# Performance work log

Hardware: AMD Instinct MI355X
Metric: run time of the kernel (lower is better)

## Reference

```python
import jax, jax.numpy as jnp
import numpy as np

D = 256          # d_model
NH = 8           # heads
NP = 4           # points per level
NL = 4           # feature levels
DH = D // NH     # head dim = 32
MLP = 4 * D      # 1024
B = 2
SHAPES = [(128, 128), (64, 64), (32, 32), (16, 16)]
LQ = sum(h * w for h, w in SHAPES)  # 21760
EPS = 1e-6


def layer_norm(x, g, b):
    mu = jnp.mean(x, axis=-1, keepdims=True)
    var = jnp.mean(jnp.square(x - mu), axis=-1, keepdims=True)
    return (x - mu) * jax.lax.rsqrt(var + EPS) * g + b


def bilinear_sample(val_l, loc, Hs, Ws):
    # val_l: [B, Hs*Ws, NH, DH]; loc: [B, Lq, NH, NP, 2] normalized in [0,1]
    v = val_l.transpose(0, 2, 1, 3)                      # [B, NH, HW, DH]
    x = loc[..., 0] * Ws - 0.5                           # [B, Lq, NH, NP]
    y = loc[..., 1] * Hs - 0.5
    x0 = jnp.floor(x); y0 = jnp.floor(y)
    lx = x - x0; ly = y - y0
    x0i = x0.astype(jnp.int32); y0i = y0.astype(jnp.int32)

    def gather(xi, yi):
        inb = (xi >= 0) & (xi < Ws) & (yi >= 0) & (yi < Hs)
        idx = jnp.clip(yi, 0, Hs - 1) * Ws + jnp.clip(xi, 0, Ws - 1)
        idx = idx.transpose(0, 2, 1, 3)                  # [B, NH, Lq, NP]
        sh = idx.shape
        idxf = idx.reshape(sh[0], sh[1], -1)
        g = jax.vmap(jax.vmap(lambda vv, ii: vv[ii]))(v, idxf)
        g = g.reshape(sh[0], sh[1], sh[2], sh[3], v.shape[-1])
        return g * inb.transpose(0, 2, 1, 3)[..., None].astype(g.dtype)

    wt = lambda a: a.transpose(0, 2, 1, 3)[..., None]    # -> [B, NH, Lq, NP, 1]
    out = (gather(x0i, y0i) * wt((1 - lx) * (1 - ly))
           + gather(x0i + 1, y0i) * wt(lx * (1 - ly))
           + gather(x0i, y0i + 1) * wt((1 - lx) * ly)
           + gather(x0i + 1, y0i + 1) * wt(lx * ly))
    return out                                            # [B, NH, Lq, NP, DH]


def setup_inputs() -> dict:
    key = jax.random.key(0)
    ks = jax.random.split(key, 16)
    ss = np.array(SHAPES, dtype=np.int64)
    lsi = np.concatenate([[0], np.cumsum(ss[:, 0] * ss[:, 1])[:-1]]).astype(np.int64)
    s = 0.02
    return {
        'src': jax.random.normal(ks[0], (B, LQ, D), jnp.float32),
        'pos': jax.random.normal(ks[1], (B, LQ, D), jnp.float32),
        'reference_points': jax.random.uniform(ks[2], (B, LQ, NL, 2), jnp.float32),
        'spatial_shapes': ss,
        'level_start_index': lsi,
        'g1': jnp.ones((D,), jnp.float32), 'beta1': jnp.zeros((D,), jnp.float32),
        'w_off': jax.random.normal(ks[3], (D, NH * NL * NP * 2), jnp.float32) * 0.01,
        'b_off': jax.random.normal(ks[4], (NH * NL * NP * 2,), jnp.float32) * 0.1,
        'w_attn': jax.random.normal(ks[5], (D, NH * NL * NP), jnp.float32) * s,
        'b_attn': jnp.zeros((NH * NL * NP,), jnp.float32),
        'w_val': jax.random.normal(ks[6], (D, D), jnp.float32) * s,
        'b_val': jnp.zeros((D,), jnp.float32),
        'w_out': jax.random.normal(ks[7], (D, D), jnp.float32) * s,
        'b_out': jnp.zeros((D,), jnp.float32),
        'g2': jnp.ones((D,), jnp.float32), 'beta2': jnp.zeros((D,), jnp.float32),
        'w_fc1': jax.random.normal(ks[8], (D, MLP), jnp.float32) * s,
        'b_fc1': jnp.zeros((MLP,), jnp.float32),
        'w_fc2': jax.random.normal(ks[9], (MLP, D), jnp.float32) * s,
        'b_fc2': jnp.zeros((D,), jnp.float32),
    }


def reference(src, pos, reference_points, spatial_shapes, level_start_index,
              g1, beta1, w_off, b_off, w_attn, b_attn, w_val, b_val,
              w_out, b_out, g2, beta2, w_fc1, b_fc1, w_fc2, b_fc2):
    ss = np.asarray(spatial_shapes)
    lsi = np.asarray(level_start_index)
    Bsz, Lq, _ = src.shape

    # --- pre-norm + multi-scale deformable attention + residual ---
    x = layer_norm(src, g1, beta1)
    q = x + pos
    val = (x @ w_val + b_val).reshape(Bsz, Lq, NH, DH)
    off = (q @ w_off + b_off).reshape(Bsz, Lq, NH, NL, NP, 2)
    aw = jax.nn.softmax((q @ w_attn + b_attn).reshape(Bsz, Lq, NH, NL * NP), axis=-1)
    aw = aw.reshape(Bsz, Lq, NH, NL, NP)

    out = jnp.zeros((Bsz, Lq, NH, DH), src.dtype)
    for l in range(NL):
        Hs, Ws = int(ss[l, 0]), int(ss[l, 1])
        start = int(lsi[l])
        vl = val[:, start:start + Hs * Ws]                       # [B, HW, NH, DH]
        norm = jnp.array([Ws, Hs], src.dtype)
        loc = reference_points[:, :, None, l, None, :] + off[:, :, :, l] / norm
        samp = bilinear_sample(vl, loc, Hs, Ws)                  # [B, NH, Lq, NP, DH]
        a = aw[:, :, :, l].transpose(0, 2, 1, 3)                 # [B, NH, Lq, NP]
        out = out + jnp.einsum('bhqp,bhqpd->bqhd', a, samp)
    attn_out = out.reshape(Bsz, Lq, D) @ w_out + b_out
    src2 = src + attn_out

    # --- pre-norm MLP + residual ---
    y = layer_norm(src2, g2, beta2)
    ffn = jax.nn.relu(y @ w_fc1 + b_fc1) @ w_fc2 + b_fc2
    return src2 + ffn
```

## Files before the change

### kernel.cpp

```cpp
#include <hip/hip_runtime.h>

#define DMODEL 256
#define NHEAD 8
#define NPOINT 4
#define NLEVEL 4
#define DHEAD 32
#define MLPD 1024
#define BSZ 2
#define LQTOK 21760
#define NTOK (BSZ * LQTOK)
#define LNEPS 1e-6f
#define FFN_CHUNK 21760

typedef __attribute__((ext_vector_type(8))) short short8;
typedef __attribute__((ext_vector_type(4))) float f32x4;

__device__ __forceinline__ float bf2f(unsigned short u) {
  unsigned int i = ((unsigned int)u) << 16;
  return __builtin_bit_cast(float, i);
}
__device__ __forceinline__ unsigned short f2bf(float f) {
  unsigned int i = __builtin_bit_cast(unsigned int, f);
  i += 0x7fff + ((i >> 16) & 1);
  return (unsigned short)(i >> 16);
}
__device__ __forceinline__ float bflo(unsigned int u) {
  return __builtin_bit_cast(float, u << 16);
}
__device__ __forceinline__ float bfhi(unsigned int u) {
  return __builtin_bit_cast(float, u & 0xffff0000u);
}

__device__ __forceinline__ void gload_lds16(const unsigned short* g,
                                            unsigned short* lds) {
  __builtin_amdgcn_global_load_lds(
      (const __attribute__((address_space(1))) unsigned int*)g,
      (__attribute__((address_space(3))) unsigned int*)lds, 16, 0, 0);
}

template <bool EMITQ>
__global__ __launch_bounds__(256) void ln_bf16(
    const float* __restrict__ in, const float* __restrict__ g,
    const float* __restrict__ beta, unsigned short* __restrict__ o,
    const float* __restrict__ pos, unsigned short* __restrict__ q) {
  const int w = threadIdx.x >> 6, lane = threadIdx.x & 63;
  const size_t t = (size_t)blockIdx.x * 4 + w;
  const size_t base = t * DMODEL + lane * 4;
  float4 v = *(const float4*)(in + base);
  float s = (v.x + v.y) + (v.z + v.w);
#pragma unroll
  for (int off = 32; off; off >>= 1) s += __shfl_xor(s, off, 64);
  float mu = s * (1.0f / DMODEL);
  float dx = v.x - mu, dy = v.y - mu, dz = v.z - mu, dw = v.w - mu;
  float s2 = (dx * dx + dy * dy) + (dz * dz + dw * dw);
#pragma unroll
  for (int off = 32; off; off >>= 1) s2 += __shfl_xor(s2, off, 64);
  float rs = rsqrtf(s2 * (1.0f / DMODEL) + LNEPS);
  float4 gg = *(const float4*)(g + lane * 4);
  float4 bb = *(const float4*)(beta + lane * 4);
  unsigned short r0 = f2bf(dx * rs * gg.x + bb.x);
  unsigned short r1 = f2bf(dy * rs * gg.y + bb.y);
  unsigned short r2 = f2bf(dz * rs * gg.z + bb.z);
  unsigned short r3 = f2bf(dw * rs * gg.w + bb.w);
  unsigned int lo = ((unsigned int)r1 << 16) | r0;
  unsigned int hi = ((unsigned int)r3 << 16) | r2;
  *(uint2*)(o + base) = make_uint2(lo, hi);
  if (EMITQ) {
    float4 p = *(const float4*)(pos + base);
    unsigned short q0 = f2bf(bf2f(r0) + p.x);
    unsigned short q1 = f2bf(bf2f(r1) + p.y);
    unsigned short q2 = f2bf(bf2f(r2) + p.z);
    unsigned short q3 = f2bf(bf2f(r3) + p.w);
    unsigned int ql = ((unsigned int)q1 << 16) | q0;
    unsigned int qh = ((unsigned int)q3 << 16) | q2;
    *(uint2*)(q + base) = make_uint2(ql, qh);
  }
}

__global__ __launch_bounds__(256) void transpose_bf16(const float* __restrict__ W,
                                                      unsigned short* __restrict__ Wt,
                                                      int K, int N) {
  __shared__ float tile[32][33];
  int k0 = blockIdx.x * 32, n0 = blockIdx.y * 32;
  int tx = threadIdx.x & 31, ty = threadIdx.x >> 5;
  for (int i = ty; i < 32; i += 8) tile[i][tx] = W[(size_t)(k0 + i) * N + n0 + tx];
  __syncthreads();
  for (int i = ty; i < 32; i += 8)
    Wt[(size_t)(n0 + i) * K + k0 + tx] = f2bf(tile[tx][i]);
}

template <int OMODE>
__global__ __launch_bounds__(256) void gemm_mfma(
    const unsigned short* __restrict__ A, const unsigned short* __restrict__ Wt,
    const float* __restrict__ bias, const float* __restrict__ res,
    void* __restrict__ Cout, int M, int N, int K) {
  __shared__ __attribute__((aligned(16))) unsigned short As[128 * 32];
  __shared__ __attribute__((aligned(16))) unsigned short Bs[128 * 32];
  const int tid = threadIdx.x;
  const int m0 = blockIdx.x * 128, n0 = blockIdx.y * 128;
  const int wave = tid >> 6, lane = tid & 63;
  const int wm = (wave & 1) * 64, wn = (wave >> 1) * 64;
  const int lr = lane & 15, quad = lane >> 4;
  f32x4 acc[4][4] = {};
  for (int k0 = 0; k0 < K; k0 += 32) {
    __syncthreads();
#pragma unroll
    for (int r = 0; r < 2; r++) {
      int c = r * 256 + tid;
      int row = c >> 2, col8 = (c & 3) * 8;
      gload_lds16(Wt + (size_t)(n0 + row) * K + k0 + col8,
                  &Bs[(r * 256 + wave * 64) * 8]);
    }
#pragma unroll
    for (int r = 0; r < 2; r++) {
      int c = r * 256 + tid;
      int row = c >> 2, col8 = (c & 3) * 8;
      gload_lds16(A + (size_t)(m0 + row) * K + k0 + col8,
                  &As[(r * 256 + wave * 64) * 8]);
    }
    __syncthreads();
    short8 af[4], bfr[4];
#pragma unroll
    for (int i = 0; i < 4; i++)
      af[i] = *(const short8*)(&As[(wm + i * 16 + lr) * 32 + quad * 8]);
#pragma unroll
    for (int j = 0; j < 4; j++)
      bfr[j] = *(const short8*)(&Bs[(wn + j * 16 + lr) * 32 + quad * 8]);
#pragma unroll
    for (int i = 0; i < 4; i++)
#pragma unroll
      for (int j = 0; j < 4; j++)
        acc[i][j] = __builtin_amdgcn_mfma_f32_16x16x32_bf16(af[i], bfr[j],
                                                            acc[i][j], 0, 0, 0);
  }
#pragma unroll
  for (int i = 0; i < 4; i++) {
    int rbase = m0 + wm + i * 16 + quad * 4;
#pragma unroll
    for (int j = 0; j < 4; j++) {
      int col = n0 + wn + j * 16 + lr;
      float bv = bias[col];
#pragma unroll
      for (int r = 0; r < 4; r++) {
        size_t idx = (size_t)(rbase + r) * N + col;
        float v = acc[i][j][r] + bv;
        if (OMODE == 2) v = fmaxf(v, 0.0f);
        if (OMODE == 3) v += res[idx];
        if (OMODE == 3)
          ((float*)Cout)[idx] = v;
        else
          ((unsigned short*)Cout)[idx] = f2bf(v);
      }
    }
  }
}

__global__ __launch_bounds__(256) void deform_sample(
    const unsigned short* __restrict__ val, const unsigned short* __restrict__ off,
    const unsigned short* __restrict__ logits, const float* __restrict__ refp,
    unsigned short* __restrict__ out) {
  __shared__ __attribute__((aligned(16))) int sIdx[4][16][8][4];
  __shared__ __attribute__((aligned(16))) float sW[4][16][8][4];
  const int w = threadIdx.x >> 6, lane = threadIdx.x & 63;
  const int bq = blockIdx.x * 4 + w;
  const int b = bq / LQTOK;
  {
    const int HW_[4] = {128, 64, 32, 16};
    const int LSI_[4] = {0, 16384, 20480, 21504};
    int u0 = 2 * lane;
    int h = u0 >> 4;
    int lvl = (u0 >> 2) & 3;
    int pt0 = u0 & 15;
    int HW = HW_[lvl];
    float2 rp = ((const float2*)refp)[(size_t)bq * 4 + lvl];
    uint2 ov = *(const uint2*)(off + (size_t)bq * 256 + 4 * lane);
    unsigned int lgu = *(const unsigned int*)(logits + (size_t)bq * 128 + 2 * lane);
    float lg0 = bflo(lgu), lg1 = bfhi(lgu);
    float mx = fmaxf(lg0, lg1);
#pragma unroll
    for (int s = 1; s < 8; s <<= 1) mx = fmaxf(mx, __shfl_xor(mx, s, 64));
    float e0 = expf(lg0 - mx), e1 = expf(lg1 - mx);
    float es = e0 + e1;
#pragma unroll
    for (int s = 1; s < 8; s <<= 1) es += __shfl_xor(es, s, 64);
    float inv = 1.0f / es;
    float a01[2] = {e0 * inv, e1 * inv};
    unsigned int ovv[2] = {ov.x, ov.y};
    int hb = h * DHEAD;
#pragma unroll
    for (int c = 0; c < 2; c++) {
      float x = fmaf(rp.x, (float)HW, bflo(ovv[c])) - 0.5f;
      float y = fmaf(rp.y, (float)HW, bfhi(ovv[c])) - 0.5f;
      float xf = floorf(x), yf = floorf(y);
      int x0 = (int)xf, y0 = (int)yf;
      float lx = x - xf, ly = y - yf;
      int x0c = min(max(x0, 0), HW - 1);
      int x1c = min(max(x0 + 1, 0), HW - 1);
      int y0c = min(max(y0, 0), HW - 1);
      int y1c = min(max(y0 + 1, 0), HW - 1);
      float m0x = (x0 >= 0 && x0 < HW) ? 1.f : 0.f;
      float m1x = (x0 + 1 >= 0 && x0 + 1 < HW) ? 1.f : 0.f;
      float m0y = (y0 >= 0 && y0 < HW) ? 1.f : 0.f;
      float m1y = (y0 + 1 >= 0 && y0 + 1 < HW) ? 1.f : 0.f;
      float a = a01[c];
      int* ip = sIdx[w][pt0 + c][h];
      float* wp = sW[w][pt0 + c][h];
      ip[0] = (LSI_[lvl] + y0c * HW + x0c) * DMODEL + hb;
      ip[1] = (LSI_[lvl] + y0c * HW + x1c) * DMODEL + hb;
      ip[2] = (LSI_[lvl] + y1c * HW + x0c) * DMODEL + hb;
      ip[3] = (LSI_[lvl] + y1c * HW + x1c) * DMODEL + hb;
      wp[0] = (1.f - lx) * (1.f - ly) * m0x * m0y * a;
      wp[1] = lx * (1.f - ly) * m1x * m0y * a;
      wp[2] = (1.f - lx) * ly * m0x * m1y * a;
      wp[3] = lx * ly * m1x * m1y * a;
    }
  }
  __builtin_amdgcn_wave_barrier();
  const int h2 = lane >> 3, g = lane & 7;
  const unsigned short* vb = val + (size_t)b * LQTOK * DMODEL + g * 4;
  float a0 = 0.f, a1 = 0.f, a2 = 0.f, a3 = 0.f;
#pragma unroll
  for (int pb = 0; pb < 4; pb++) {
    int4 ix[4];
    float4 wt[4];
#pragma unroll
    for (int p = 0; p < 4; p++) {
      ix[p] = *(const int4*)sIdx[w][pb * 4 + p][h2];
      wt[p] = *(const float4*)sW[w][pb * 4 + p][h2];
    }
    uint2 v4[4][4];
#pragma unroll
    for (int p = 0; p < 4; p++) {
      v4[p][0] = *(const uint2*)(vb + ix[p].x);
      v4[p][1] = *(const uint2*)(vb + ix[p].y);
      v4[p][2] = *(const uint2*)(vb + ix[p].z);
      v4[p][3] = *(const uint2*)(vb + ix[p].w);
    }
#pragma unroll
    for (int p = 0; p < 4; p++) {
      float wk[4] = {wt[p].x, wt[p].y, wt[p].z, wt[p].w};
#pragma unroll
      for (int k = 0; k < 4; k++) {
        uint2 u = v4[p][k];
        a0 = fmaf(wk[k], bflo(u.x), a0);
        a1 = fmaf(wk[k], bfhi(u.x), a1);
        a2 = fmaf(wk[k], bflo(u.y), a2);
        a3 = fmaf(wk[k], bfhi(u.y), a3);
      }
    }
  }
  unsigned int o0 = ((unsigned int)f2bf(a1) << 16) | f2bf(a0);
  unsigned int o1 = ((unsigned int)f2bf(a3) << 16) | f2bf(a2);
  *(uint2*)(out + (size_t)bq * 256 + h2 * 32 + g * 4) = make_uint2(o0, o1);
}

extern "C" void kernel_launch(void* const* d_in, const int* in_sizes, int n_in,
                              void* d_out, int out_size, void* d_ws,
                              size_t ws_size, hipStream_t stream) {
  const float* src    = (const float*)d_in[0];
  const float* pos    = (const float*)d_in[1];
  const float* refp   = (const float*)d_in[2];
  const float* g1     = (const float*)d_in[5];
  const float* beta1  = (const float*)d_in[6];
  const float* w_off  = (const float*)d_in[7];
  const float* b_off  = (const float*)d_in[8];
  const float* w_attn = (const float*)d_in[9];
  const float* b_attn = (const float*)d_in[10];
  const float* w_val  = (const float*)d_in[11];
  const float* b_val  = (const float*)d_in[12];
  const float* w_out  = (const float*)d_in[13];
  const float* b_out  = (const float*)d_in[14];
  const float* g2     = (const float*)d_in[15];
  const float* beta2  = (const float*)d_in[16];
  const float* w_fc1  = (const float*)d_in[17];
  const float* b_fc1  = (const float*)d_in[18];
  const float* w_fc2  = (const float*)d_in[19];
  const float* b_fc2  = (const float*)d_in[20];
  float* out = (float*)d_out;

  const size_t NT = (size_t)NTOK;
  unsigned short* b1 = (unsigned short*)d_ws;
  unsigned short* b2 = b1 + NT * 256;
  unsigned short* b3 = b2 + NT * 256;
  float* b4 = (float*)(b3 + NT * 256);
  float* b5 = b4 + NT * 128;
  unsigned short* wvalT  = (unsigned short*)(b5 + NT * 256);
  unsigned short* woffT  = wvalT + 256 * 256;
  unsigned short* wattnT = woffT + 256 * 256;
  unsigned short* woutT  = wattnT + 128 * 256;
  unsigned short* wfc1T  = woutT + 256 * 256;
  unsigned short* wfc2T  = wfc1T + 1024 * 256;

  unsigned short* qb  = (unsigned short*)b4;
  unsigned short* lgb = (unsigned short*)b5;

  transpose_bf16<<<dim3(8, 8), 256, 0, stream>>>(w_val, wvalT, 256, 256);
  transpose_bf16<<<dim3(8, 8), 256, 0, stream>>>(w_off, woffT, 256, 256);
  transpose_bf16<<<dim3(8, 4), 256, 0, stream>>>(w_attn, wattnT, 256, 128);
  transpose_bf16<<<dim3(8, 8), 256, 0, stream>>>(w_out, woutT, 256, 256);
  transpose_bf16<<<dim3(8, 32), 256, 0, stream>>>(w_fc1, wfc1T, 256, 1024);
  transpose_bf16<<<dim3(32, 8), 256, 0, stream>>>(w_fc2, wfc2T, 1024, 256);

  const int MT = NTOK / 128;

  ln_bf16<true><<<NTOK / 4, 256, 0, stream>>>(src, g1, beta1, b1, pos, qb);
  gemm_mfma<1><<<dim3(MT, 2), 256, 0, stream>>>(b1, wvalT, b_val, nullptr, b2,
                                                NTOK, 256, 256);
  gemm_mfma<1><<<dim3(MT, 2), 256, 0, stream>>>(qb, woffT, b_off, nullptr, b3,
                                                NTOK, 256, 256);
  gemm_mfma<1><<<dim3(MT, 1), 256, 0, stream>>>(qb, wattnT, b_attn, nullptr,
                                                lgb, NTOK, 128, 256);
  deform_sample<<<NTOK / 4, 256, 0, stream>>>(b2, b3, lgb, refp, b1);
  gemm_mfma<3><<<dim3(MT, 2), 256, 0, stream>>>(b1, woutT, b_out, src, b5,
                                                NTOK, 256, 256);
  ln_bf16<false><<<NTOK / 4, 256, 0, stream>>>(b5, g2, beta2, b3, nullptr,
                                               nullptr);
  unsigned short* hid = b1;
  for (int c = 0; c < 2; c++) {
    size_t ro = (size_t)c * FFN_CHUNK;
    gemm_mfma<2><<<dim3(FFN_CHUNK / 128, 8), 256, 0, stream>>>(
        b3 + ro * 256, wfc1T, b_fc1, nullptr, hid, FFN_CHUNK, 1024, 256);
    gemm_mfma<3><<<dim3(FFN_CHUNK / 128, 2), 256, 0, stream>>>(
        hid, wfc2T, b_fc2, b5 + ro * 256, out + ro * 256, FFN_CHUNK, 256, 1024);
  }
}
```

Baseline: 475.7 us.

## Fuse offset/attn GEMMs, swizzle sample LDS, packed FMA, unchunk FFN

```diff
diff --git a/kernel.cpp b/kernel.cpp
--- a/kernel.cpp
+++ b/kernel.cpp
@@ -10,10 +10,10 @@
 #define LQTOK 21760
 #define NTOK (BSZ * LQTOK)
 #define LNEPS 1e-6f
-#define FFN_CHUNK 21760
 
 typedef __attribute__((ext_vector_type(8))) short short8;
 typedef __attribute__((ext_vector_type(4))) float f32x4;
+typedef __attribute__((ext_vector_type(2))) float f32x2;
 
 __device__ __forceinline__ float bf2f(unsigned short u) {
   unsigned int i = ((unsigned int)u) << 16;
@@ -29,6 +29,13 @@
 }
 __device__ __forceinline__ float bfhi(unsigned int u) {
   return __builtin_bit_cast(float, u & 0xffff0000u);
+}
+
+__device__ __forceinline__ void pk_fma_bcast(f32x2& d, f32x2 a, float b) {
+  f32x2 bb;
+  bb[0] = b;
+  bb[1] = b;
+  asm("v_pk_fma_f32 %0, %1, %2, %0" : "+v"(d) : "v"(a), "v"(bb));
 }
 
 __device__ __forceinline__ void gload_lds16(const unsigned short* g,
@@ -93,7 +100,7 @@
 __global__ __launch_bounds__(256) void gemm_mfma(
     const unsigned short* __restrict__ A, const unsigned short* __restrict__ Wt,
     const float* __restrict__ bias, const float* __restrict__ res,
-    void* __restrict__ Cout, int M, int N, int K) {
+    void* __restrict__ Cout, void* __restrict__ Cout2, int M, int N, int K) {
   __shared__ __attribute__((aligned(16))) unsigned short As[128 * 32];
   __shared__ __attribute__((aligned(16))) unsigned short Bs[128 * 32];
   const int tid = threadIdx.x;
@@ -139,17 +146,25 @@
 #pragma unroll
     for (int j = 0; j < 4; j++) {
       int col = n0 + wn + j * 16 + lr;
-      float bv = bias[col];
+      float bv = (OMODE == 4 && col >= 256) ? res[col - 256] : bias[col];
 #pragma unroll
       for (int r = 0; r < 4; r++) {
-        size_t idx = (size_t)(rbase + r) * N + col;
         float v = acc[i][j][r] + bv;
         if (OMODE == 2) v = fmaxf(v, 0.0f);
-        if (OMODE == 3) v += res[idx];
-        if (OMODE == 3)
-          ((float*)Cout)[idx] = v;
-        else
-          ((unsigned short*)Cout)[idx] = f2bf(v);
+        if (OMODE == 4) {
+          size_t row = (size_t)(rbase + r);
+          if (col < 256)
+            ((unsigned short*)Cout)[row * 256 + col] = f2bf(v);
+          else
+            ((unsigned short*)Cout2)[row * 128 + (col - 256)] = f2bf(v);
+        } else {
+          size_t idx = (size_t)(rbase + r) * N + col;
+          if (OMODE == 3) {
+            ((float*)Cout)[idx] = v + res[idx];
+          } else {
+            ((unsigned short*)Cout)[idx] = f2bf(v);
+          }
+        }
       }
     }
   }
@@ -163,7 +178,7 @@
   __shared__ __attribute__((aligned(16))) float sW[4][16][8][4];
   const int w = threadIdx.x >> 6, lane = threadIdx.x & 63;
   const int bq = blockIdx.x * 4 + w;
-  const int b = bq / LQTOK;
+  const int b = __builtin_amdgcn_readfirstlane(bq / LQTOK);
   {
     const int HW_[4] = {128, 64, 32, 16};
     const int LSI_[4] = {0, 16384, 20480, 21504};
@@ -186,7 +201,7 @@
     float inv = 1.0f / es;
     float a01[2] = {e0 * inv, e1 * inv};
     unsigned int ovv[2] = {ov.x, ov.y};
-    int hb = h * DHEAD;
+    int hb2 = h * (DHEAD * 2);
 #pragma unroll
     for (int c = 0; c < 2; c++) {
       float x = fmaf(rp.x, (float)HW, bflo(ovv[c])) - 0.5f;
@@ -203,54 +218,63 @@
       float m0y = (y0 >= 0 && y0 < HW) ? 1.f : 0.f;
       float m1y = (y0 + 1 >= 0 && y0 + 1 < HW) ? 1.f : 0.f;
       float a = a01[c];
-      int* ip = sIdx[w][pt0 + c][h];
-      float* wp = sW[w][pt0 + c][h];
-      ip[0] = (LSI_[lvl] + y0c * HW + x0c) * DMODEL + hb;
-      ip[1] = (LSI_[lvl] + y0c * HW + x1c) * DMODEL + hb;
-      ip[2] = (LSI_[lvl] + y1c * HW + x0c) * DMODEL + hb;
-      ip[3] = (LSI_[lvl] + y1c * HW + x1c) * DMODEL + hb;
-      wp[0] = (1.f - lx) * (1.f - ly) * m0x * m0y * a;
-      wp[1] = lx * (1.f - ly) * m1x * m0y * a;
-      wp[2] = (1.f - lx) * ly * m0x * m1y * a;
-      wp[3] = lx * ly * m1x * m1y * a;
+      int pt = pt0 + c;
+      int hs = h ^ (pt & 7);
+      int r0 = (LSI_[lvl] + y0c * HW) * (DMODEL * 2) + hb2;
+      int r1 = (LSI_[lvl] + y1c * HW) * (DMODEL * 2) + hb2;
+      *(int4*)sIdx[w][pt][hs] =
+          make_int4(r0 + x0c * (DMODEL * 2), r0 + x1c * (DMODEL * 2),
+                    r1 + x0c * (DMODEL * 2), r1 + x1c * (DMODEL * 2));
+      *(float4*)sW[w][pt][hs] =
+          make_float4((1.f - lx) * (1.f - ly) * m0x * m0y * a,
+                      lx * (1.f - ly) * m1x * m0y * a,
+                      (1.f - lx) * ly * m0x * m1y * a,
+                      lx * ly * m1x * m1y * a);
     }
   }
   __builtin_amdgcn_wave_barrier();
   const int h2 = lane >> 3, g = lane & 7;
-  const unsigned short* vb = val + (size_t)b * LQTOK * DMODEL + g * 4;
-  float a0 = 0.f, a1 = 0.f, a2 = 0.f, a3 = 0.f;
+  const char* basep =
+      (const char*)val + (size_t)b * ((size_t)LQTOK * DMODEL * 2);
+  const int goff = g * 8;
+  f32x2 a01v = {0.f, 0.f}, a23v = {0.f, 0.f};
 #pragma unroll
   for (int pb = 0; pb < 4; pb++) {
     int4 ix[4];
-    float4 wt[4];
+    float4 wt4[4];
 #pragma unroll
     for (int p = 0; p < 4; p++) {
-      ix[p] = *(const int4*)sIdx[w][pb * 4 + p][h2];
-      wt[p] = *(const float4*)sW[w][pb * 4 + p][h2];
+      int pt = pb * 4 + p;
+      int hs = h2 ^ (pt & 7);
+      ix[p] = *(const int4*)sIdx[w][pt][hs];
+      wt4[p] = *(const float4*)sW[w][pt][hs];
     }
     uint2 v4[4][4];
 #pragma unroll
     for (int p = 0; p < 4; p++) {
-      v4[p][0] = *(const uint2*)(vb + ix[p].x);
-      v4[p][1] = *(const uint2*)(vb + ix[p].y);
-      v4[p][2] = *(const uint2*)(vb + ix[p].z);
-      v4[p][3] = *(const uint2*)(vb + ix[p].w);
+      v4[p][0] = *(const uint2*)(basep + (unsigned)(ix[p].x + goff));
+      v4[p][1] = *(const uint2*)(basep + (unsigned)(ix[p].y + goff));
+      v4[p][2] = *(const uint2*)(basep + (unsigned)(ix[p].z + goff));
+      v4[p][3] = *(const uint2*)(basep + (unsigned)(ix[p].w + goff));
     }
 #pragma unroll
     for (int p = 0; p < 4; p++) {
-      float wk[4] = {wt[p].x, wt[p].y, wt[p].z, wt[p].w};
+      float wk[4] = {wt4[p].x, wt4[p].y, wt4[p].z, wt4[p].w};
 #pragma unroll
       for (int k = 0; k < 4; k++) {
         uint2 u = v4[p][k];
-        a0 = fmaf(wk[k], bflo(u.x), a0);
-        a1 = fmaf(wk[k], bfhi(u.x), a1);
-        a2 = fmaf(wk[k], bflo(u.y), a2);
-        a3 = fmaf(wk[k], bfhi(u.y), a3);
+        f32x2 vlo, vhi;
+        vlo[0] = bflo(u.x);
+        vlo[1] = bfhi(u.x);
+        vhi[0] = bflo(u.y);
+        vhi[1] = bfhi(u.y);
+        pk_fma_bcast(a01v, vlo, wk[k]);
+        pk_fma_bcast(a23v, vhi, wk[k]);
       }
     }
   }
-  unsigned int o0 = ((unsigned int)f2bf(a1) << 16) | f2bf(a0);
-  unsigned int o1 = ((unsigned int)f2bf(a3) << 16) | f2bf(a2);
+  unsigned int o0 = ((unsigned int)f2bf(a01v[1]) << 16) | f2bf(a01v[0]);
+  unsigned int o1 = ((unsigned int)f2bf(a23v[1]) << 16) | f2bf(a23v[0]);
   *(uint2*)(out + (size_t)bq * 256 + h2 * 32 + g * 4) = make_uint2(o0, o1);
 }
 
@@ -282,21 +306,23 @@
   unsigned short* b1 = (unsigned short*)d_ws;
   unsigned short* b2 = b1 + NT * 256;
   unsigned short* b3 = b2 + NT * 256;
-  float* b4 = (float*)(b3 + NT * 256);
-  float* b5 = b4 + NT * 128;
-  unsigned short* wvalT  = (unsigned short*)(b5 + NT * 256);
-  unsigned short* woffT  = wvalT + 256 * 256;
-  unsigned short* wattnT = woffT + 256 * 256;
-  unsigned short* woutT  = wattnT + 128 * 256;
+  unsigned short* b4 = b3 + NT * 256;
+  unsigned short* b5 = b4 + NT * 256;
+  unsigned short* wvalT  = b5 + NT * 512;
+  unsigned short* woffaT = wvalT + 256 * 256;
+  unsigned short* woutT  = woffaT + 384 * 256;
   unsigned short* wfc1T  = woutT + 256 * 256;
   unsigned short* wfc2T  = wfc1T + 1024 * 256;
 
-  unsigned short* qb  = (unsigned short*)b4;
-  unsigned short* lgb = (unsigned short*)b5;
+  unsigned short* qb  = b4;
+  unsigned short* lgb = b5;
+  unsigned short* yb  = b5;
+  unsigned short* hid = b1;
 
   transpose_bf16<<<dim3(8, 8), 256, 0, stream>>>(w_val, wvalT, 256, 256);
-  transpose_bf16<<<dim3(8, 8), 256, 0, stream>>>(w_off, woffT, 256, 256);
-  transpose_bf16<<<dim3(8, 4), 256, 0, stream>>>(w_attn, wattnT, 256, 128);
+  transpose_bf16<<<dim3(8, 8), 256, 0, stream>>>(w_off, woffaT, 256, 256);
+  transpose_bf16<<<dim3(8, 4), 256, 0, stream>>>(w_attn, woffaT + 256 * 256,
+                                                 256, 128);
   transpose_bf16<<<dim3(8, 8), 256, 0, stream>>>(w_out, woutT, 256, 256);
   transpose_bf16<<<dim3(8, 32), 256, 0, stream>>>(w_fc1, wfc1T, 256, 1024);
   transpose_bf16<<<dim3(32, 8), 256, 0, stream>>>(w_fc2, wfc2T, 1024, 256);
@@ -305,22 +331,16 @@
 
   ln_bf16<true><<<NTOK / 4, 256, 0, stream>>>(src, g1, beta1, b1, pos, qb);
   gemm_mfma<1><<<dim3(MT, 2), 256, 0, stream>>>(b1, wvalT, b_val, nullptr, b2,
-                                                NTOK, 256, 256);
-  gemm_mfma<1><<<dim3(MT, 2), 256, 0, stream>>>(qb, woffT, b_off, nullptr, b3,
-                                                NTOK, 256, 256);
-  gemm_mfma<1><<<dim3(MT, 1), 256, 0, stream>>>(qb, wattnT, b_attn, nullptr,
-                                                lgb, NTOK, 128, 256);
+                                                nullptr, NTOK, 256, 256);
+  gemm_mfma<4><<<dim3(MT, 3), 256, 0, stream>>>(qb, woffaT, b_off, b_attn, b3,
+                                                lgb, NTOK, 384, 256);
   deform_sample<<<NTOK / 4, 256, 0, stream>>>(b2, b3, lgb, refp, b1);
-  gemm_mfma<3><<<dim3(MT, 2), 256, 0, stream>>>(b1, woutT, b_out, src, b5,
-                                                NTOK, 256, 256);
-  ln_bf16<false><<<NTOK / 4, 256, 0, stream>>>(b5, g2, beta2, b3, nullptr,
+  gemm_mfma<3><<<dim3(MT, 2), 256, 0, stream>>>(b1, woutT, b_out, src, out,
+                                                nullptr, NTOK, 256, 256);
+  ln_bf16<false><<<NTOK / 4, 256, 0, stream>>>(out, g2, beta2, yb, nullptr,
                                                nullptr);
-  unsigned short* hid = b1;
-  for (int c = 0; c < 2; c++) {
-    size_t ro = (size_t)c * FFN_CHUNK;
-    gemm_mfma<2><<<dim3(FFN_CHUNK / 128, 8), 256, 0, stream>>>(
-        b3 + ro * 256, wfc1T, b_fc1, nullptr, hid, FFN_CHUNK, 1024, 256);
-    gemm_mfma<3><<<dim3(FFN_CHUNK / 128, 2), 256, 0, stream>>>(
-        hid, wfc2T, b_fc2, b5 + ro * 256, out + ro * 256, FFN_CHUNK, 256, 1024);
-  }
-}
+  gemm_mfma<2><<<dim3(MT, 8), 256, 0, stream>>>(yb, wfc1T, b_fc1, nullptr, hid,
+                                                nullptr, NTOK, 1024, 256);
+  gemm_mfma<3><<<dim3(MT, 2), 256, 0, stream>>>(hid, wfc2T, b_fc2, out, out,
+                                                nullptr, NTOK, 256, 1024);
+}
```

Result: faster. 445.8 us (-6.3%).
